# Kernel tuning notes

Measured on AMD Instinct MI355X. Metric: run time of the kernel, lower is better.

## Reference

```python
import jax, jax.numpy as jnp
import numpy as np

N = 50000      # nodes
E = 800000     # edges (avg degree 16)
D = 128        # feature / channel width (channel_counts=[128,128,128])
HEAD = 64      # head_dim
NEG_SLOPE = 0.2  # PyG GATConv leaky_relu slope


def setup_inputs() -> dict:
    key = jax.random.key(0)
    ks = jax.random.split(key, 32)
    s = 1.0 / np.sqrt(D)

    def w(k, shape):
        return jax.random.normal(k, shape, jnp.float32) * s

    return {
        "x": jax.random.normal(ks[0], (N, D), jnp.float32),
        "edge_index": jax.random.randint(ks[1], (2, E), 0, N, dtype=jnp.int32),
        # layer 0: lazy (-1,-1) GATConv -> separate src/dst linear maps
        "w0_src": w(ks[2], (D, D)), "w0_dst": w(ks[3], (D, D)),
        "a0_src": w(ks[4], (D,)), "a0_dst": w(ks[5], (D,)),
        "bc0": jnp.zeros((D,), jnp.float32),
        "wl0": w(ks[6], (D, D)), "bl0": jnp.zeros((D,), jnp.float32),
        # layer 1: int in_channels -> shared weight
        "w1": w(ks[7], (D, D)),
        "a1_src": w(ks[8], (D,)), "a1_dst": w(ks[9], (D,)),
        "bc1": jnp.zeros((D,), jnp.float32),
        "wl1": w(ks[10], (D, D)), "bl1": jnp.zeros((D,), jnp.float32),
        # layer 2
        "w2": w(ks[11], (D, D)),
        "a2_src": w(ks[12], (D,)), "a2_dst": w(ks[13], (D,)),
        "bc2": jnp.zeros((D,), jnp.float32),
        "wl2": w(ks[14], (D, D)), "bl2": jnp.zeros((D,), jnp.float32),
        # head linear
        "wh": w(ks[15], (D, HEAD)), "bh": jnp.zeros((HEAD,), jnp.float32),
    }


def _gat(h_src, h_dst, src, dst, a_src, a_dst, bias):
    """PyG GATConv (heads=1, no self loops, eval-mode). h_*: [N,C]."""
    al_s = h_src @ a_src                                   # [N]
    al_d = h_dst @ a_dst                                   # [N]
    logits = jax.nn.leaky_relu(al_s[src] + al_d[dst], NEG_SLOPE)  # [E]
    m = jax.ops.segment_max(logits, dst, num_segments=N)  # per-dest max
    e = jnp.exp(logits - m[dst])
    denom = jax.ops.segment_sum(e, dst, num_segments=N)
    alpha = e / denom[dst]                                 # [E]
    msg = h_src[src] * alpha[:, None]                      # [E,C]
    return jax.ops.segment_sum(msg, dst, num_segments=N) + bias


def reference(x, edge_index, w0_src, w0_dst, a0_src, a0_dst, bc0, wl0, bl0,
              w1, a1_src, a1_dst, bc1, wl1, bl1,
              w2, a2_src, a2_dst, bc2, wl2, bl2, wh, bh):
    src, dst = edge_index[0], edge_index[1]
    # layer 0: conv(x) + lin(x), relu
    h = _gat(x @ w0_src, x @ w0_dst, src, dst, a0_src, a0_dst, bc0) + x @ wl0 + bl0
    h = jax.nn.relu(h)
    # layer 1: shared-weight conv
    hs = h @ w1
    h = _gat(hs, hs, src, dst, a1_src, a1_dst, bc1) + h @ wl1 + bl1
    h = jax.nn.relu(h)
    # layer 2 (no relu)
    hs = h @ w2
    h = _gat(hs, hs, src, dst, a2_src, a2_dst, bc2) + h @ wl2 + bl2
    # head
    return h @ wh + bh
```

## Files before the change

### kernel.cpp

```cpp
#include <hip/hip_runtime.h>

#define NNODE 50000
#define NEDGE 800000
#define DIM   128
#define NEG   0.2f
#define NBUCK 196
#define EPB1  2048
#define NB1   391
#define GBLK  782
#define GN    12500
#define SB_PA (NB1)
#define SB_PH (SB_PA + 32)
#define SB_MV (SB_PH + 9)
#define SB_CV (SB_MV + 193)
#define SB_TOT (SB_CV + GN)

typedef __attribute__((ext_vector_type(8))) short bf16x8;
typedef __attribute__((ext_vector_type(4))) float f32x4;

__device__ __forceinline__ float wmax(float v){
  #pragma unroll
  for (int m = 32; m > 0; m >>= 1) v = fmaxf(v, __shfl_xor(v, m));
  return v;
}
__device__ __forceinline__ float wsum(float v){
  #pragma unroll
  for (int m = 32; m > 0; m >>= 1) v += __shfl_xor(v, m);
  return v;
}
__device__ __forceinline__ unsigned short f2bf(float f){
  unsigned int x = __float_as_uint(f);
  return (unsigned short)((x + 0x7fffu + ((x >> 16) & 1u)) >> 16);
}
__device__ __forceinline__ float bflo(unsigned u){ return __uint_as_float(u << 16); }
__device__ __forceinline__ float bfhi(unsigned u){ return __uint_as_float(u & 0xffff0000u); }

__global__ __launch_bounds__(256) void setup_k(
    const int* __restrict__ ei,
    const float* __restrict__ x,
    const float* __restrict__ w0s, const float* __restrict__ a0s,
    const float* __restrict__ w0d, const float* __restrict__ a0d,
    const float* __restrict__ bc0, const float* __restrict__ wl0,
    const float* __restrict__ bl0,
    const float* __restrict__ w1,  const float* __restrict__ a1s,
    const float* __restrict__ a1d, const float* __restrict__ bc1,
    const float* __restrict__ wl1, const float* __restrict__ bl1,
    const float* __restrict__ w2,  const float* __restrict__ a2s,
    const float* __restrict__ a2d, const float* __restrict__ bc2,
    const float* __restrict__ wl2, const float* __restrict__ bl2,
    const float* __restrict__ wh,  const float* __restrict__ bh,
    int* __restrict__ cnt,
    unsigned short* __restrict__ Wz1, unsigned short* __restrict__ Wz2,
    unsigned short* __restrict__ Wz3, float* __restrict__ bf3,
    float* __restrict__ uv, float* __restrict__ bf1, float* __restrict__ bf2,
    unsigned int* __restrict__ Xb){
  int bid = blockIdx.x;

  if (bid < NB1){
    __shared__ int h[NBUCK];
    const int* dst = ei + NEDGE;
    for (int i = threadIdx.x; i < NBUCK; i += 256) h[i] = 0;
    __syncthreads();
    int e0 = bid * EPB1 + threadIdx.x;
    #pragma unroll
    for (int i = 0; i < 8; ++i){
      int e = e0 + i * 256;
      if (e < NEDGE) atomicAdd(&h[dst[e] >> 8], 1);
    }
    __syncthreads();
    for (int i = threadIdx.x; i < NBUCK; i += 256)
      cnt[i * NB1 + bid] = h[i];
    return;
  }
  if (bid < SB_PH){
    int g = (bid - SB_PA) * 256 + threadIdx.x;
    int layer = g >> 12;
    int rem = g & 4095;
    int ct = rem >> 9, q = (rem >> 6) & 7, lane = rem & 63;
    int quad = lane >> 4;
    int c = ct * 16 + (lane & 15);
    const float* wA = layer ? w1 : w0s;
    const float* wB = layer ? wl1 : wl0;
    unsigned short* dst = (layer ? Wz2 : Wz1) + ((size_t)(ct * 8 + q) * 64 + lane) * 8;
    #pragma unroll
    for (int j = 0; j < 8; ++j){
      int k = q * 32 + quad * 8 + j;
      float v = (k < 128) ? wA[k * 128 + c] : wB[(k - 128) * 128 + c];
      dst[j] = f2bf(v);
    }
    return;
  }
  if (bid < SB_MV){
    int pb = bid - SB_PH;
    if (pb == 8){
      int c = threadIdx.x;
      if (c < 64){
        float s = bh[c];
        for (int t = 0; t < 128; ++t) s += (bc2[t] + bl2[t]) * wh[t * 64 + c];
        bf3[c] = s;
      }
      return;
    }
    int g = pb * 256 + threadIdx.x;
    int ct = g >> 9, q = (g >> 6) & 7, lane = g & 63;
    int quad = lane >> 4;
    int c = ct * 16 + (lane & 15);
    unsigned short* dst = Wz3 + ((size_t)(ct * 8 + q) * 64 + lane) * 8;
    #pragma unroll
    for (int j = 0; j < 8; ++j){
      int k = q * 32 + quad * 8 + j;
      const float* src = (k < 128) ? (w2 + k * 128) : (wl2 + (k - 128) * 128);
      float s = 0.f;
      for (int t = 0; t < 128; ++t) s += src[t] * wh[t * 64 + c];
      dst[j] = f2bf(s);
    }
    return;
  }
  if (bid < SB_CV){
    int mb = bid - SB_MV;
    if (mb == 192){
      int t = threadIdx.x;
      if (t < 128) bf1[t] = bc0[t] + bl0[t];
      else bf2[t - 128] = bc1[t - 128] + bl1[t - 128];
      return;
    }
    int lane = threadIdx.x & 63;
    int idx = mb * 4 + (threadIdx.x >> 6);
    int grp = idx >> 7, r = idx & 127;
    const float* W; const float* a;
    switch (grp){
      case 0: W = w0s; a = a0s; break;
      case 1: W = w0d; a = a0d; break;
      case 2: W = w1;  a = a1s; break;
      case 3: W = w1;  a = a1d; break;
      case 4: W = w2;  a = a2s; break;
      default: W = w2; a = a2d; break;
    }
    float2 w = ((const float2*)(W + r * DIM))[lane];
    float2 av = ((const float2*)a)[lane];
    float s = wsum(w.x * av.x + w.y * av.y);
    if (lane == 0) uv[grp * 128 + r] = s;
    return;
  }
  {
    int lane = threadIdx.x & 63;
    int n = (bid - SB_CV) * 4 + (threadIdx.x >> 6);
    if (n >= NNODE) return;
    float2 xv = ((const float2*)(x + (size_t)n * DIM))[lane];
    Xb[(size_t)n * 64 + lane] = (unsigned)f2bf(xv.x) | ((unsigned)f2bf(xv.y) << 16);
  }
}

__global__ __launch_bounds__(256) void scan196_k(const int* __restrict__ cnt,
                                                 int* __restrict__ cbase,
                                                 int* __restrict__ btot){
  __shared__ int sd[256];
  int b = blockIdx.x, t = threadIdx.x;
  const int* row = cnt + (size_t)b * NB1;
  int i0 = t * 2, i1 = t * 2 + 1;
  int v0 = (i0 < NB1) ? row[i0] : 0;
  int v1 = (i1 < NB1) ? row[i1] : 0;
  int s = v0 + v1;
  sd[t] = s; __syncthreads();
  #pragma unroll
  for (int off = 1; off < 256; off <<= 1){
    int u = (t >= off) ? sd[t - off] : 0;
    __syncthreads();
    sd[t] += u;
    __syncthreads();
  }
  int ex = sd[t] - s;
  if (i0 < NB1) cbase[(size_t)b * NB1 + i0] = ex;
  if (i1 < NB1) cbase[(size_t)b * NB1 + i1] = ex + v0;
  if (t == 255) btot[b] = sd[255];
}

__global__ __launch_bounds__(256) void bscan2_k(const int* __restrict__ btot,
                                                int* __restrict__ gbase,
                                                int* __restrict__ rp,
                                                const float* __restrict__ X,
                                                const float* __restrict__ uv,
                                                float* __restrict__ als,
                                                float* __restrict__ ald){
  if (blockIdx.x > 0){
    int lane = threadIdx.x & 63;
    int n = (blockIdx.x - 1) * 4 + (threadIdx.x >> 6);
    if (n >= NNODE) return;
    float2 xv = ((const float2*)(X + (size_t)n * DIM))[lane];
    float2 uu = ((const float2*)uv)[lane];
    float2 vv = ((const float2*)(uv + 128))[lane];
    float s1 = wsum(xv.x * uu.x + xv.y * uu.y);
    float s2 = wsum(xv.x * vv.x + xv.y * vv.y);
    if (lane == 0){ als[n] = s1; ald[n] = s2; }
    return;
  }
  __shared__ int sd[256];
  int t = threadIdx.x;
  int v = (t < NBUCK) ? btot[t] : 0;
  sd[t] = v; __syncthreads();
  #pragma unroll
  for (int off = 1; off < 256; off <<= 1){
    int u = (t >= off) ? sd[t - off] : 0;
    __syncthreads();
    sd[t] += u;
    __syncthreads();
  }
  if (t < NBUCK) gbase[t] = sd[t] - v;
  if (t == NBUCK - 1) gbase[NBUCK] = sd[t];
  if (t == 0) rp[NNODE] = NEDGE;
}

__global__ __launch_bounds__(256) void scat2_k(const int* __restrict__ ei,
                                               const int* __restrict__ gbase,
                                               const int* __restrict__ cbase,
                                               unsigned int* __restrict__ packed){
  __shared__ int lcur[NBUCK];
  for (int i = threadIdx.x; i < NBUCK; i += 256) lcur[i] = 0;
  __syncthreads();
  int e0 = blockIdx.x * EPB1 + threadIdx.x;
  #pragma unroll
  for (int i = 0; i < 8; ++i){
    int e = e0 + i * 256;
    if (e < NEDGE){
      int s = ei[e], d = ei[NEDGE + e];
      int b = d >> 8;
      int r = atomicAdd(&lcur[b], 1);
      int pos = gbase[b] + cbase[(size_t)b * NB1 + blockIdx.x] + r;
      packed[pos] = ((unsigned)d << 16) | (unsigned)s;
    }
  }
}

__global__ __launch_bounds__(256) void build_k(const int* __restrict__ gbase,
                                               const unsigned int* __restrict__ packed,
                                               int* __restrict__ rp,
                                               unsigned short* __restrict__ es){
  __shared__ int h[256], sd[256], cur[256];
  int b = blockIdx.x, t = threadIdx.x;
  int s0 = gbase[b], s1 = gbase[b + 1];
  h[t] = 0; __syncthreads();
  for (int i = s0 + t; i < s1; i += 256)
    atomicAdd(&h[(packed[i] >> 16) & 255], 1);
  __syncthreads();
  int v = h[t]; sd[t] = v; __syncthreads();
  #pragma unroll
  for (int off = 1; off < 256; off <<= 1){
    int u = (t >= off) ? sd[t - off] : 0;
    __syncthreads();
    sd[t] += u;
    __syncthreads();
  }
  int ex = sd[t] - v;
  cur[t] = ex;
  int d = b * 256 + t;
  if (d < NNODE) rp[d] = s0 + ex;
  __syncthreads();
  for (int i = s0 + t; i < s1; i += 256){
    unsigned int p = packed[i];
    int ld = (p >> 16) & 255;
    int pos = atomicAdd(&cur[ld], 1);
    es[s0 + pos] = (unsigned short)(p & 0xffffu);
  }
}

__global__ __launch_bounds__(256) void gat_k(const int* __restrict__ rp,
                                             const unsigned short* __restrict__ es,
                                             const float* __restrict__ als,
                                             const float* __restrict__ ald,
                                             const unsigned int* __restrict__ A,
                                             unsigned int* __restrict__ Mb){
  int lane = threadIdx.x & 63;
  int n = blockIdx.x * 4 + (threadIdx.x >> 6);
  if (n >= NNODE) return;
  int start = rp[n], end = rp[n + 1];
  int deg = end - start;
  float ad = ald[n];

  if (deg <= 64){
    int s = 0; float z = -3.0e38f;
    if (lane < deg){
      s = es[start + lane];
      float t = als[s] + ad;
      z = t > 0.f ? t : NEG * t;
    }
    float m = wmax(z);
    float e = (lane < deg) ? __expf(z - m) : 0.f;
    float denom = wsum(e);
    float rinv = (deg > 0) ? 1.f / denom : 0.f;

    int half = lane >> 4;
    int sub  = lane & 15;
    const uint4* A4 = (const uint4*)A;
    float a0 = 0.f, a1 = 0.f, a2 = 0.f, a3 = 0.f;
    float a4 = 0.f, a5 = 0.f, a6 = 0.f, a7 = 0.f;
    int dq = (deg + 7) & ~7;
    for (int j = 0; j < dq; j += 8){
      int   sA = __shfl(s, j + half);
      int   sB = __shfl(s, j + 4 + half);
      float wA = __shfl(e, j + half);
      float wB = __shfl(e, j + 4 + half);
      uint4 pA = A4[(size_t)sA * 16 + sub];
      uint4 pB = A4[(size_t)sB * 16 + sub];
      a0 = fmaf(wA, bflo(pA.x), a0); a1 = fmaf(wA, bfhi(pA.x), a1);
      a2 = fmaf(wA, bflo(pA.y), a2); a3 = fmaf(wA, bfhi(pA.y), a3);
      a4 = fmaf(wA, bflo(pA.z), a4); a5 = fmaf(wA, bfhi(pA.z), a5);
      a6 = fmaf(wA, bflo(pA.w), a6); a7 = fmaf(wA, bfhi(pA.w), a7);
      a0 = fmaf(wB, bflo(pB.x), a0); a1 = fmaf(wB, bfhi(pB.x), a1);
      a2 = fmaf(wB, bflo(pB.y), a2); a3 = fmaf(wB, bfhi(pB.y), a3);
      a4 = fmaf(wB, bflo(pB.z), a4); a5 = fmaf(wB, bfhi(pB.z), a5);
      a6 = fmaf(wB, bflo(pB.w), a6); a7 = fmaf(wB, bfhi(pB.w), a7);
    }
    #define RED(v) v += __shfl_xor(v, 16); v += __shfl_xor(v, 32);
    RED(a0) RED(a1) RED(a2) RED(a3) RED(a4) RED(a5) RED(a6) RED(a7)
    #undef RED
    if (half == 0){
      uint4 o;
      o.x = (unsigned)f2bf(a0 * rinv) | ((unsigned)f2bf(a1 * rinv) << 16);
      o.y = (unsigned)f2bf(a2 * rinv) | ((unsigned)f2bf(a3 * rinv) << 16);
      o.z = (unsigned)f2bf(a4 * rinv) | ((unsigned)f2bf(a5 * rinv) << 16);
      o.w = (unsigned)f2bf(a6 * rinv) | ((unsigned)f2bf(a7 * rinv) << 16);
      ((uint4*)(Mb + (size_t)n * 64))[sub] = o;
    }
  } else {
    float2 acc = make_float2(0.f, 0.f);
    float mloc = -3.0e38f;
    for (int i = start + lane; i < end; i += 64){
      int s = es[i];
      float zz = als[s] + ad;
      zz = zz > 0.f ? zz : NEG * zz;
      mloc = fmaxf(mloc, zz);
    }
    float m = wmax(mloc);
    float dloc = 0.f;
    for (int i = start + lane; i < end; i += 64){
      int s = es[i];
      float zz = als[s] + ad;
      zz = zz > 0.f ? zz : NEG * zz;
      dloc += __expf(zz - m);
    }
    float rinv = 1.f / wsum(dloc);
    for (int i = start; i < end; ++i){
      int s = es[i];
      float zz = als[s] + ad;
      zz = zz > 0.f ? zz : NEG * zz;
      float w = __expf(zz - m);
      unsigned p = A[(size_t)s * 64 + lane];
      acc.x = fmaf(w, bflo(p), acc.x);
      acc.y = fmaf(w, bfhi(p), acc.y);
    }
    Mb[(size_t)n * 64 + lane] =
        (unsigned)f2bf(acc.x * rinv) | ((unsigned)f2bf(acc.y * rinv) << 16);
  }
}

template<int FINAL>
__global__ __launch_bounds__(256) void mfma_k(const unsigned int* __restrict__ Mb,
                                              const unsigned int* __restrict__ Hin,
                                              const unsigned short* __restrict__ Wz,
                                              const float* __restrict__ bias,
                                              const float* __restrict__ u,
                                              const float* __restrict__ v,
                                              unsigned short* __restrict__ Hout,
                                              float* __restrict__ outf,
                                              float* __restrict__ als,
                                              float* __restrict__ ald){
  int lane = threadIdx.x & 63;
  int wid  = threadIdx.x >> 6;
  int r0   = blockIdx.x * 64 + wid * 16;
  int quad = lane >> 4;
  int col  = lane & 15;

  int rA = r0 + col; if (rA > NNODE - 1) rA = NNODE - 1;
  const bf16x8* mrow = (const bf16x8*)(Mb + (size_t)rA * 64);
  const bf16x8* hrow = (const bf16x8*)(Hin + (size_t)rA * 64);
  bf16x8 a[8];
  #pragma unroll
  for (int q = 0; q < 4; ++q){
    a[q]     = mrow[q * 4 + quad];
    a[q + 4] = hrow[q * 4 + quad];
  }

  const bf16x8* wz = (const bf16x8*)Wz;
  int rowq = r0 + quad * 4;
  float alsp[4] = {0.f, 0.f, 0.f, 0.f};
  float aldp[4] = {0.f, 0.f, 0.f, 0.f};
  const int NCT = FINAL ? 4 : 8;

  #pragma unroll
  for (int ct = 0; ct < NCT; ++ct){
    f32x4 acc = {0.f, 0.f, 0.f, 0.f};
    #pragma unroll
    for (int q = 0; q < 8; ++q){
      bf16x8 bfr = wz[(ct * 8 + q) * 64 + lane];
      acc = __builtin_amdgcn_mfma_f32_16x16x32_bf16(a[q], bfr, acc, 0, 0, 0);
    }
    int c = ct * 16 + col;
    float bb = bias[c];
    if (FINAL){
      #pragma unroll
      for (int r = 0; r < 4; ++r){
        int row = rowq + r;
        if (row < NNODE) outf[(size_t)row * 64 + c] = acc[r] + bb;
      }
    } else {
      float uc = u[c], vc = v[c];
      #pragma unroll
      for (int r = 0; r < 4; ++r){
        float h = fmaxf(acc[r] + bb, 0.f);
        alsp[r] = fmaf(h, uc, alsp[r]);
        aldp[r] = fmaf(h, vc, aldp[r]);
        int row = rowq + r;
        if (row < NNODE) Hout[(size_t)row * 128 + c] = f2bf(h);
      }
    }
  }

  if (!FINAL){
    #pragma unroll
    for (int m = 1; m < 16; m <<= 1){
      #pragma unroll
      for (int r = 0; r < 4; ++r){
        alsp[r] += __shfl_xor(alsp[r], m);
        aldp[r] += __shfl_xor(aldp[r], m);
      }
    }
    if (col == 0){
      #pragma unroll
      for (int r = 0; r < 4; ++r){
        int row = rowq + r;
        if (row < NNODE){ als[row] = alsp[r]; ald[row] = aldp[r]; }
      }
    }
  }
}

extern "C" void kernel_launch(void* const* d_in, const int* in_sizes, int n_in,
                              void* d_out, int out_size, void* d_ws, size_t ws_size,
                              hipStream_t stream){
  const float* x   = (const float*)d_in[0];
  const int*   ei  = (const int*)d_in[1];
  const float* w0s = (const float*)d_in[2];
  const float* w0d = (const float*)d_in[3];
  const float* a0s = (const float*)d_in[4];
  const float* a0d = (const float*)d_in[5];
  const float* bc0 = (const float*)d_in[6];
  const float* wl0 = (const float*)d_in[7];
  const float* bl0 = (const float*)d_in[8];
  const float* w1  = (const float*)d_in[9];
  const float* a1s = (const float*)d_in[10];
  const float* a1d = (const float*)d_in[11];
  const float* bc1 = (const float*)d_in[12];
  const float* wl1 = (const float*)d_in[13];
  const float* bl1 = (const float*)d_in[14];
  const float* w2  = (const float*)d_in[15];
  const float* a2s = (const float*)d_in[16];
  const float* a2d = (const float*)d_in[17];
  const float* bc2 = (const float*)d_in[18];
  const float* wl2 = (const float*)d_in[19];
  const float* bl2 = (const float*)d_in[20];
  const float* wh  = (const float*)d_in[21];
  const float* bh  = (const float*)d_in[22];
  float* out = (float*)d_out;

  unsigned int* Xb = (unsigned int*)d_ws;
  unsigned int* Ha = Xb + (size_t)NNODE * 64;
  unsigned int* Hb = Ha + (size_t)NNODE * 64;
  unsigned int* Mb = Hb + (size_t)NNODE * 64;
  float* alsA = (float*)(Mb + (size_t)NNODE * 64);
  float* aldA = alsA + NNODE;
  float* alsB = aldA + NNODE;
  float* aldB = alsB + NNODE;
  float* uv   = aldB + NNODE;
  float* bf1  = uv + 6 * 128;
  float* bf2  = bf1 + 128;
  float* bf3  = bf2 + 128;
  unsigned short* Wz1 = (unsigned short*)(bf3 + 64);
  unsigned short* Wz2 = Wz1 + 256 * 128;
  unsigned short* Wz3 = Wz2 + 256 * 128;
  int*   rp    = (int*)(Wz3 + 256 * 64);
  int*   cnt   = rp + (NNODE + 1);
  int*   cbase = cnt + NBUCK * NB1;
  int*   btot  = cbase + NBUCK * NB1;
  int*   gbase = btot + NBUCK;
  unsigned int* packed = (unsigned int*)(gbase + (NBUCK + 1));
  unsigned short* es   = (unsigned short*)(packed + NEDGE);

  dim3 b(256);
  dim3 gn(GN);

  setup_k<<<SB_TOT, b, 0, stream>>>(ei, x,
      w0s, a0s, w0d, a0d, bc0, wl0, bl0,
      w1, a1s, a1d, bc1, wl1, bl1,
      w2, a2s, a2d, bc2, wl2, bl2, wh, bh,
      cnt, Wz1, Wz2, Wz3, bf3, uv, bf1, bf2, Xb);

  scan196_k<<<NBUCK, b, 0, stream>>>(cnt, cbase, btot);
  bscan2_k<<<1 + GN, b, 0, stream>>>(btot, gbase, rp, x, uv, alsA, aldA);
  scat2_k<<<NB1, b, 0, stream>>>(ei, gbase, cbase, packed);
  build_k<<<NBUCK, b, 0, stream>>>(gbase, packed, rp, es);

  gat_k<<<gn, b, 0, stream>>>(rp, es, alsA, aldA, Xb, Mb);
  mfma_k<0><<<GBLK, b, 0, stream>>>(Mb, Xb, Wz1, bf1, uv + 2 * 128, uv + 3 * 128,
                                    (unsigned short*)Ha, nullptr, alsB, aldB);

  gat_k<<<gn, b, 0, stream>>>(rp, es, alsB, aldB, Ha, Mb);
  mfma_k<0><<<GBLK, b, 0, stream>>>(Mb, Ha, Wz2, bf2, uv + 4 * 128, uv + 5 * 128,
                                    (unsigned short*)Hb, nullptr, alsA, aldA);

  gat_k<<<gn, b, 0, stream>>>(rp, es, alsA, aldA, Hb, Mb);
  mfma_k<1><<<GBLK, b, 0, stream>>>(Mb, Hb, Wz3, bf3, nullptr, nullptr,
                                    nullptr, out, nullptr, nullptr);
}
```

Measured before the change: 307.0 us.

## Split GAT aggregation into alpha pass and column-strip gather with strip-major features

Node features are stored strip-major, as four column strips of 32 bf16 per node, so each strip's gather working set is a quarter of the full feature table. The softmax weights are computed once per layer into a per-edge alpha buffer that reuses the packed scratch area. A new kernel then gathers one strip per block over a four-fold larger grid. The aim is better L2 locality for the random source-row gathers. The cost is an extra kernel launch per layer, four re-reads of edge indices and alpha, and scattered strided writes in the mfma epilogue.

```diff
diff --git a/kernel.cpp b/kernel.cpp
--- a/kernel.cpp
+++ b/kernel.cpp
@@ -9,6 +9,8 @@
 #define NB1   391
 #define GBLK  782
 #define GN    12500
+#define NSTRIP 4
+#define SDW   (NNODE * 16)
 #define SB_PA (NB1)
 #define SB_PH (SB_PA + 32)
 #define SB_MV (SB_PH + 9)
@@ -147,7 +149,8 @@
     int n = (bid - SB_CV) * 4 + (threadIdx.x >> 6);
     if (n >= NNODE) return;
     float2 xv = ((const float2*)(x + (size_t)n * DIM))[lane];
-    Xb[(size_t)n * 64 + lane] = (unsigned)f2bf(xv.x) | ((unsigned)f2bf(xv.y) << 16);
+    unsigned pk = (unsigned)f2bf(xv.x) | ((unsigned)f2bf(xv.y) << 16);
+    Xb[(size_t)(lane >> 4) * SDW + (size_t)n * 16 + (lane & 15)] = pk;
   }
 }
 
@@ -263,66 +266,32 @@
   }
 }
 
-__global__ __launch_bounds__(256) void gat_k(const int* __restrict__ rp,
-                                             const unsigned short* __restrict__ es,
-                                             const float* __restrict__ als,
-                                             const float* __restrict__ ald,
-                                             const unsigned int* __restrict__ A,
-                                             unsigned int* __restrict__ Mb){
+__global__ __launch_bounds__(256) void alpha_k(const int* __restrict__ rp,
+                                               const unsigned short* __restrict__ es,
+                                               const float* __restrict__ als,
+                                               const float* __restrict__ ald,
+                                               float* __restrict__ alpha){
   int lane = threadIdx.x & 63;
   int n = blockIdx.x * 4 + (threadIdx.x >> 6);
   if (n >= NNODE) return;
   int start = rp[n], end = rp[n + 1];
   int deg = end - start;
+  if (deg == 0) return;
   float ad = ald[n];
 
   if (deg <= 64){
-    int s = 0; float z = -3.0e38f;
+    float z = -3.0e38f;
+    int idx = start + lane;
     if (lane < deg){
-      s = es[start + lane];
+      int s = es[idx];
       float t = als[s] + ad;
       z = t > 0.f ? t : NEG * t;
     }
     float m = wmax(z);
     float e = (lane < deg) ? __expf(z - m) : 0.f;
-    float denom = wsum(e);
-    float rinv = (deg > 0) ? 1.f / denom : 0.f;
-
-    int half = lane >> 4;
-    int sub  = lane & 15;
-    const uint4* A4 = (const uint4*)A;
-    float a0 = 0.f, a1 = 0.f, a2 = 0.f, a3 = 0.f;
-    float a4 = 0.f, a5 = 0.f, a6 = 0.f, a7 = 0.f;
-    int dq = (deg + 7) & ~7;
-    for (int j = 0; j < dq; j += 8){
-      int   sA = __shfl(s, j + half);
-      int   sB = __shfl(s, j + 4 + half);
-      float wA = __shfl(e, j + half);
-      float wB = __shfl(e, j + 4 + half);
-      uint4 pA = A4[(size_t)sA * 16 + sub];
-      uint4 pB = A4[(size_t)sB * 16 + sub];
-      a0 = fmaf(wA, bflo(pA.x), a0); a1 = fmaf(wA, bfhi(pA.x), a1);
-      a2 = fmaf(wA, bflo(pA.y), a2); a3 = fmaf(wA, bfhi(pA.y), a3);
-      a4 = fmaf(wA, bflo(pA.z), a4); a5 = fmaf(wA, bfhi(pA.z), a5);
-      a6 = fmaf(wA, bflo(pA.w), a6); a7 = fmaf(wA, bfhi(pA.w), a7);
-      a0 = fmaf(wB, bflo(pB.x), a0); a1 = fmaf(wB, bfhi(pB.x), a1);
-      a2 = fmaf(wB, bflo(pB.y), a2); a3 = fmaf(wB, bfhi(pB.y), a3);
-      a4 = fmaf(wB, bflo(pB.z), a4); a5 = fmaf(wB, bfhi(pB.z), a5);
-      a6 = fmaf(wB, bflo(pB.w), a6); a7 = fmaf(wB, bfhi(pB.w), a7);
-    }
-    #define RED(v) v += __shfl_xor(v, 16); v += __shfl_xor(v, 32);
-    RED(a0) RED(a1) RED(a2) RED(a3) RED(a4) RED(a5) RED(a6) RED(a7)
-    #undef RED
-    if (half == 0){
-      uint4 o;
-      o.x = (unsigned)f2bf(a0 * rinv) | ((unsigned)f2bf(a1 * rinv) << 16);
-      o.y = (unsigned)f2bf(a2 * rinv) | ((unsigned)f2bf(a3 * rinv) << 16);
-      o.z = (unsigned)f2bf(a4 * rinv) | ((unsigned)f2bf(a5 * rinv) << 16);
-      o.w = (unsigned)f2bf(a6 * rinv) | ((unsigned)f2bf(a7 * rinv) << 16);
-      ((uint4*)(Mb + (size_t)n * 64))[sub] = o;
-    }
+    float rinv = 1.f / wsum(e);
+    if (lane < deg) alpha[idx] = e * rinv;
   } else {
-    float2 acc = make_float2(0.f, 0.f);
     float mloc = -3.0e38f;
     for (int i = start + lane; i < end; i += 64){
       int s = es[i];
@@ -339,18 +308,48 @@
       dloc += __expf(zz - m);
     }
     float rinv = 1.f / wsum(dloc);
-    for (int i = start; i < end; ++i){
+    for (int i = start + lane; i < end; i += 64){
       int s = es[i];
       float zz = als[s] + ad;
       zz = zz > 0.f ? zz : NEG * zz;
-      float w = __expf(zz - m);
-      unsigned p = A[(size_t)s * 64 + lane];
-      acc.x = fmaf(w, bflo(p), acc.x);
-      acc.y = fmaf(w, bfhi(p), acc.y);
-    }
-    Mb[(size_t)n * 64 + lane] =
-        (unsigned)f2bf(acc.x * rinv) | ((unsigned)f2bf(acc.y * rinv) << 16);
-  }
+      alpha[i] = __expf(zz - m) * rinv;
+    }
+  }
+}
+
+__global__ __launch_bounds__(256) void mgat_k(const int* __restrict__ rp,
+                                              const unsigned short* __restrict__ es,
+                                              const float* __restrict__ alpha,
+                                              const unsigned int* __restrict__ A,
+                                              unsigned int* __restrict__ Mb){
+  int bid = blockIdx.x;
+  int strip = bid / GN;
+  int nb = bid - strip * GN;
+  int lane = threadIdx.x & 63;
+  int n = nb * 4 + (threadIdx.x >> 6);
+  if (n >= NNODE) return;
+  int start = rp[n], end = rp[n + 1];
+  int half = lane >> 4, sub = lane & 15;
+  const unsigned int* As = A + (size_t)strip * SDW;
+  float ax = 0.f, ay = 0.f;
+
+  for (int j = start; j < end; j += 8){
+    int i0 = j + half, i1 = j + 4 + half;
+    bool v0 = i0 < end, v1 = i1 < end;
+    int s0 = v0 ? es[i0] : 0;
+    int s1 = v1 ? es[i1] : 0;
+    float w0 = v0 ? alpha[i0] : 0.f;
+    float w1 = v1 ? alpha[i1] : 0.f;
+    unsigned p0 = As[(size_t)s0 * 16 + sub];
+    unsigned p1 = As[(size_t)s1 * 16 + sub];
+    ax = fmaf(w0, bflo(p0), ax); ay = fmaf(w0, bfhi(p0), ay);
+    ax = fmaf(w1, bflo(p1), ax); ay = fmaf(w1, bfhi(p1), ay);
+  }
+  ax += __shfl_xor(ax, 16); ax += __shfl_xor(ax, 32);
+  ay += __shfl_xor(ay, 16); ay += __shfl_xor(ay, 32);
+  if (half == 0)
+    Mb[(size_t)strip * SDW + (size_t)n * 16 + sub] =
+        (unsigned)f2bf(ax) | ((unsigned)f2bf(ay) << 16);
 }
 
 template<int FINAL>
@@ -371,13 +370,13 @@
   int col  = lane & 15;
 
   int rA = r0 + col; if (rA > NNODE - 1) rA = NNODE - 1;
-  const bf16x8* mrow = (const bf16x8*)(Mb + (size_t)rA * 64);
-  const bf16x8* hrow = (const bf16x8*)(Hin + (size_t)rA * 64);
+  const unsigned int* mb = Mb  + (size_t)rA * 16 + quad * 4;
+  const unsigned int* hb = Hin + (size_t)rA * 16 + quad * 4;
   bf16x8 a[8];
   #pragma unroll
   for (int q = 0; q < 4; ++q){
-    a[q]     = mrow[q * 4 + quad];
-    a[q + 4] = hrow[q * 4 + quad];
+    a[q]     = *(const bf16x8*)(mb + (size_t)q * SDW);
+    a[q + 4] = *(const bf16x8*)(hb + (size_t)q * SDW);
   }
 
   const bf16x8* wz = (const bf16x8*)Wz;
@@ -410,7 +409,8 @@
         alsp[r] = fmaf(h, uc, alsp[r]);
         aldp[r] = fmaf(h, vc, aldp[r]);
         int row = rowq + r;
-        if (row < NNODE) Hout[(size_t)row * 128 + c] = f2bf(h);
+        if (row < NNODE)
+          Hout[(size_t)(c >> 5) * (NNODE * 32) + (size_t)row * 32 + (c & 31)] = f2bf(h);
       }
     }
   }
@@ -484,9 +484,11 @@
   int*   gbase = btot + NBUCK;
   unsigned int* packed = (unsigned int*)(gbase + (NBUCK + 1));
   unsigned short* es   = (unsigned short*)(packed + NEDGE);
+  float* alpha = (float*)packed;
 
   dim3 b(256);
   dim3 gn(GN);
+  dim3 gs(NSTRIP * GN);
 
   setup_k<<<SB_TOT, b, 0, stream>>>(ei, x,
       w0s, a0s, w0d, a0d, bc0, wl0, bl0,
@@ -499,15 +501,18 @@
   scat2_k<<<NB1, b, 0, stream>>>(ei, gbase, cbase, packed);
   build_k<<<NBUCK, b, 0, stream>>>(gbase, packed, rp, es);
 
-  gat_k<<<gn, b, 0, stream>>>(rp, es, alsA, aldA, Xb, Mb);
+  alpha_k<<<gn, b, 0, stream>>>(rp, es, alsA, aldA, alpha);
+  mgat_k<<<gs, b, 0, stream>>>(rp, es, alpha, Xb, Mb);
   mfma_k<0><<<GBLK, b, 0, stream>>>(Mb, Xb, Wz1, bf1, uv + 2 * 128, uv + 3 * 128,
                                     (unsigned short*)Ha, nullptr, alsB, aldB);
 
-  gat_k<<<gn, b, 0, stream>>>(rp, es, alsB, aldB, Ha, Mb);
+  alpha_k<<<gn, b, 0, stream>>>(rp, es, alsB, aldB, alpha);
+  mgat_k<<<gs, b, 0, stream>>>(rp, es, alpha, Ha, Mb);
   mfma_k<0><<<GBLK, b, 0, stream>>>(Mb, Ha, Wz2, bf2, uv + 4 * 128, uv + 5 * 128,
                                     (unsigned short*)Hb, nullptr, alsA, aldA);
 
-  gat_k<<<gn, b, 0, stream>>>(rp, es, alsA, aldA, Hb, Mb);
+  alpha_k<<<gn, b, 0, stream>>>(rp, es, alsA, aldA, alpha);
+  mgat_k<<<gs, b, 0, stream>>>(rp, es, alpha, Hb, Mb);
   mfma_k<1><<<GBLK, b, 0, stream>>>(Mb, Hb, Wz3, bf3, nullptr, nullptr,
                                     nullptr, out, nullptr, nullptr);
 }
```

Result: slower. 499.0 us (+62.5%).

## Fuse GAT aggregation into MFMA transform kernel via swizzled LDS staging

Applied to the files above, without the earlier changes.

Merges the per-node attention aggregation kernel into the following MFMA linear kernel. Each wave now aggregates its 16 rows, writes the bf16 results into XOR-swizzled shared memory, and reads them back as MFMA A fragments, so the Mb intermediate no longer goes through global memory and three launches disappear. In exchange the grid drops from 12500 to 782 blocks, and each wave handles 16 nodes one after another. This cuts parallelism available for hiding gather latency and may worsen load imbalance.

```diff
diff --git a/kernel.cpp b/kernel.cpp
--- a/kernel.cpp
+++ b/kernel.cpp
@@ -263,120 +263,110 @@
   }
 }
 
-__global__ __launch_bounds__(256) void gat_k(const int* __restrict__ rp,
-                                             const unsigned short* __restrict__ es,
-                                             const float* __restrict__ als,
-                                             const float* __restrict__ ald,
-                                             const unsigned int* __restrict__ A,
-                                             unsigned int* __restrict__ Mb){
-  int lane = threadIdx.x & 63;
-  int n = blockIdx.x * 4 + (threadIdx.x >> 6);
-  if (n >= NNODE) return;
-  int start = rp[n], end = rp[n + 1];
-  int deg = end - start;
-  float ad = ald[n];
-
-  if (deg <= 64){
-    int s = 0; float z = -3.0e38f;
-    if (lane < deg){
-      s = es[start + lane];
-      float t = als[s] + ad;
-      z = t > 0.f ? t : NEG * t;
-    }
-    float m = wmax(z);
-    float e = (lane < deg) ? __expf(z - m) : 0.f;
-    float denom = wsum(e);
-    float rinv = (deg > 0) ? 1.f / denom : 0.f;
-
-    int half = lane >> 4;
-    int sub  = lane & 15;
-    const uint4* A4 = (const uint4*)A;
-    float a0 = 0.f, a1 = 0.f, a2 = 0.f, a3 = 0.f;
-    float a4 = 0.f, a5 = 0.f, a6 = 0.f, a7 = 0.f;
-    int dq = (deg + 7) & ~7;
-    for (int j = 0; j < dq; j += 8){
-      int   sA = __shfl(s, j + half);
-      int   sB = __shfl(s, j + 4 + half);
-      float wA = __shfl(e, j + half);
-      float wB = __shfl(e, j + 4 + half);
-      uint4 pA = A4[(size_t)sA * 16 + sub];
-      uint4 pB = A4[(size_t)sB * 16 + sub];
-      a0 = fmaf(wA, bflo(pA.x), a0); a1 = fmaf(wA, bfhi(pA.x), a1);
-      a2 = fmaf(wA, bflo(pA.y), a2); a3 = fmaf(wA, bfhi(pA.y), a3);
-      a4 = fmaf(wA, bflo(pA.z), a4); a5 = fmaf(wA, bfhi(pA.z), a5);
-      a6 = fmaf(wA, bflo(pA.w), a6); a7 = fmaf(wA, bfhi(pA.w), a7);
-      a0 = fmaf(wB, bflo(pB.x), a0); a1 = fmaf(wB, bfhi(pB.x), a1);
-      a2 = fmaf(wB, bflo(pB.y), a2); a3 = fmaf(wB, bfhi(pB.y), a3);
-      a4 = fmaf(wB, bflo(pB.z), a4); a5 = fmaf(wB, bfhi(pB.z), a5);
-      a6 = fmaf(wB, bflo(pB.w), a6); a7 = fmaf(wB, bfhi(pB.w), a7);
-    }
-    #define RED(v) v += __shfl_xor(v, 16); v += __shfl_xor(v, 32);
-    RED(a0) RED(a1) RED(a2) RED(a3) RED(a4) RED(a5) RED(a6) RED(a7)
-    #undef RED
-    if (half == 0){
-      uint4 o;
-      o.x = (unsigned)f2bf(a0 * rinv) | ((unsigned)f2bf(a1 * rinv) << 16);
-      o.y = (unsigned)f2bf(a2 * rinv) | ((unsigned)f2bf(a3 * rinv) << 16);
-      o.z = (unsigned)f2bf(a4 * rinv) | ((unsigned)f2bf(a5 * rinv) << 16);
-      o.w = (unsigned)f2bf(a6 * rinv) | ((unsigned)f2bf(a7 * rinv) << 16);
-      ((uint4*)(Mb + (size_t)n * 64))[sub] = o;
-    }
-  } else {
-    float2 acc = make_float2(0.f, 0.f);
-    float mloc = -3.0e38f;
-    for (int i = start + lane; i < end; i += 64){
-      int s = es[i];
-      float zz = als[s] + ad;
-      zz = zz > 0.f ? zz : NEG * zz;
-      mloc = fmaxf(mloc, zz);
-    }
-    float m = wmax(mloc);
-    float dloc = 0.f;
-    for (int i = start + lane; i < end; i += 64){
-      int s = es[i];
-      float zz = als[s] + ad;
-      zz = zz > 0.f ? zz : NEG * zz;
-      dloc += __expf(zz - m);
-    }
-    float rinv = 1.f / wsum(dloc);
-    for (int i = start; i < end; ++i){
-      int s = es[i];
-      float zz = als[s] + ad;
-      zz = zz > 0.f ? zz : NEG * zz;
-      float w = __expf(zz - m);
-      unsigned p = A[(size_t)s * 64 + lane];
-      acc.x = fmaf(w, bflo(p), acc.x);
-      acc.y = fmaf(w, bfhi(p), acc.y);
-    }
-    Mb[(size_t)n * 64 + lane] =
-        (unsigned)f2bf(acc.x * rinv) | ((unsigned)f2bf(acc.y * rinv) << 16);
-  }
-}
-
 template<int FINAL>
-__global__ __launch_bounds__(256) void mfma_k(const unsigned int* __restrict__ Mb,
-                                              const unsigned int* __restrict__ Hin,
-                                              const unsigned short* __restrict__ Wz,
-                                              const float* __restrict__ bias,
-                                              const float* __restrict__ u,
-                                              const float* __restrict__ v,
-                                              unsigned short* __restrict__ Hout,
-                                              float* __restrict__ outf,
-                                              float* __restrict__ als,
-                                              float* __restrict__ ald){
+__global__ __launch_bounds__(256) void fused_k(
+    const int* __restrict__ rp, const unsigned short* __restrict__ es,
+    const float* __restrict__ alsi, const float* __restrict__ aldi,
+    const unsigned int* __restrict__ A,
+    const unsigned int* __restrict__ Hin,
+    const unsigned short* __restrict__ Wz,
+    const float* __restrict__ bias,
+    const float* __restrict__ u, const float* __restrict__ v,
+    unsigned short* __restrict__ Hout, float* __restrict__ outf,
+    float* __restrict__ also, float* __restrict__ aldo){
+  __shared__ unsigned int lds[64 * 64];
   int lane = threadIdx.x & 63;
   int wid  = threadIdx.x >> 6;
   int r0   = blockIdx.x * 64 + wid * 16;
-  int quad = lane >> 4;
-  int col  = lane & 15;
-
+  int half = lane >> 4, sub = lane & 15;
+  const uint4* A4 = (const uint4*)A;
+  uint4* lds4 = (uint4*)lds;
+
+  for (int i = 0; i < 16; ++i){
+    int n = r0 + i;
+    if (n >= NNODE) break;
+    int start = rp[n], end = rp[n + 1];
+    int deg = end - start;
+    float ad = aldi[n];
+    if (deg <= 64){
+      int s = 0; float z = -3.0e38f;
+      if (lane < deg){
+        s = es[start + lane];
+        float t = alsi[s] + ad;
+        z = t > 0.f ? t : NEG * t;
+      }
+      float m = wmax(z);
+      float e = (lane < deg) ? __expf(z - m) : 0.f;
+      float denom = wsum(e);
+      float rinv = (deg > 0) ? 1.f / denom : 0.f;
+      float a0=0.f,a1=0.f,a2=0.f,a3=0.f,a4=0.f,a5=0.f,a6=0.f,a7=0.f;
+      int dq = (deg + 7) & ~7;
+      for (int j = 0; j < dq; j += 8){
+        int   sA = __shfl(s, j + half);
+        int   sB = __shfl(s, j + 4 + half);
+        float wA = __shfl(e, j + half);
+        float wB = __shfl(e, j + 4 + half);
+        uint4 pA = A4[(size_t)sA * 16 + sub];
+        uint4 pB = A4[(size_t)sB * 16 + sub];
+        a0 = fmaf(wA, bflo(pA.x), a0); a1 = fmaf(wA, bfhi(pA.x), a1);
+        a2 = fmaf(wA, bflo(pA.y), a2); a3 = fmaf(wA, bfhi(pA.y), a3);
+        a4 = fmaf(wA, bflo(pA.z), a4); a5 = fmaf(wA, bfhi(pA.z), a5);
+        a6 = fmaf(wA, bflo(pA.w), a6); a7 = fmaf(wA, bfhi(pA.w), a7);
+        a0 = fmaf(wB, bflo(pB.x), a0); a1 = fmaf(wB, bfhi(pB.x), a1);
+        a2 = fmaf(wB, bflo(pB.y), a2); a3 = fmaf(wB, bfhi(pB.y), a3);
+        a4 = fmaf(wB, bflo(pB.z), a4); a5 = fmaf(wB, bfhi(pB.z), a5);
+        a6 = fmaf(wB, bflo(pB.w), a6); a7 = fmaf(wB, bfhi(pB.w), a7);
+      }
+      #define RED(vv) vv += __shfl_xor(vv, 16); vv += __shfl_xor(vv, 32);
+      RED(a0) RED(a1) RED(a2) RED(a3) RED(a4) RED(a5) RED(a6) RED(a7)
+      #undef RED
+      if (half == 0){
+        uint4 o;
+        o.x = (unsigned)f2bf(a0 * rinv) | ((unsigned)f2bf(a1 * rinv) << 16);
+        o.y = (unsigned)f2bf(a2 * rinv) | ((unsigned)f2bf(a3 * rinv) << 16);
+        o.z = (unsigned)f2bf(a4 * rinv) | ((unsigned)f2bf(a5 * rinv) << 16);
+        o.w = (unsigned)f2bf(a6 * rinv) | ((unsigned)f2bf(a7 * rinv) << 16);
+        lds4[(wid * 16 + i) * 16 + (sub ^ (i & 7))] = o;
+      }
+    } else {
+      float mloc = -3.0e38f;
+      for (int it = start + lane; it < end; it += 64){
+        int s = es[it];
+        float zz = alsi[s] + ad;
+        zz = zz > 0.f ? zz : NEG * zz;
+        mloc = fmaxf(mloc, zz);
+      }
+      float m = wmax(mloc);
+      float dloc = 0.f;
+      for (int it = start + lane; it < end; it += 64){
+        int s = es[it];
+        float zz = alsi[s] + ad;
+        zz = zz > 0.f ? zz : NEG * zz;
+        dloc += __expf(zz - m);
+      }
+      float rinv = 1.f / wsum(dloc);
+      float ax = 0.f, ay = 0.f;
+      for (int it = start; it < end; ++it){
+        int s = es[it];
+        float zz = alsi[s] + ad;
+        zz = zz > 0.f ? zz : NEG * zz;
+        float w = __expf(zz - m);
+        unsigned p = A[(size_t)s * 64 + lane];
+        ax = fmaf(w, bflo(p), ax);
+        ay = fmaf(w, bfhi(p), ay);
+      }
+      lds[(wid * 16 + i) * 64 + (lane ^ ((i & 7) << 2))] =
+          (unsigned)f2bf(ax * rinv) | ((unsigned)f2bf(ay * rinv) << 16);
+    }
+  }
+
+  int quad = half, col = sub;
   int rA = r0 + col; if (rA > NNODE - 1) rA = NNODE - 1;
-  const bf16x8* mrow = (const bf16x8*)(Mb + (size_t)rA * 64);
   const bf16x8* hrow = (const bf16x8*)(Hin + (size_t)rA * 64);
   bf16x8 a[8];
   #pragma unroll
   for (int q = 0; q < 4; ++q){
-    a[q]     = mrow[q * 4 + quad];
+    a[q]     = *(const bf16x8*)&lds4[(wid * 16 + col) * 16 + ((q * 4 + quad) ^ (col & 7))];
     a[q + 4] = hrow[q * 4 + quad];
   }
 
@@ -428,7 +418,7 @@
       #pragma unroll
       for (int r = 0; r < 4; ++r){
         int row = rowq + r;
-        if (row < NNODE){ als[row] = alsp[r]; ald[row] = aldp[r]; }
+        if (row < NNODE){ also[row] = alsp[r]; aldo[row] = aldp[r]; }
       }
     }
   }
@@ -486,7 +476,6 @@
   unsigned short* es   = (unsigned short*)(packed + NEDGE);
 
   dim3 b(256);
-  dim3 gn(GN);
 
   setup_k<<<SB_TOT, b, 0, stream>>>(ei, x,
       w0s, a0s, w0d, a0d, bc0, wl0, bl0,
@@ -499,15 +488,15 @@
   scat2_k<<<NB1, b, 0, stream>>>(ei, gbase, cbase, packed);
   build_k<<<NBUCK, b, 0, stream>>>(gbase, packed, rp, es);
 
-  gat_k<<<gn, b, 0, stream>>>(rp, es, alsA, aldA, Xb, Mb);
-  mfma_k<0><<<GBLK, b, 0, stream>>>(Mb, Xb, Wz1, bf1, uv + 2 * 128, uv + 3 * 128,
-                                    (unsigned short*)Ha, nullptr, alsB, aldB);
-
-  gat_k<<<gn, b, 0, stream>>>(rp, es, alsB, aldB, Ha, Mb);
-  mfma_k<0><<<GBLK, b, 0, stream>>>(Mb, Ha, Wz2, bf2, uv + 4 * 128, uv + 5 * 128,
-                                    (unsigned short*)Hb, nullptr, alsA, aldA);
-
-  gat_k<<<gn, b, 0, stream>>>(rp, es, alsA, aldA, Hb, Mb);
-  mfma_k<1><<<GBLK, b, 0, stream>>>(Mb, Hb, Wz3, bf3, nullptr, nullptr,
-                                    nullptr, out, nullptr, nullptr);
-}
+  fused_k<0><<<GBLK, b, 0, stream>>>(rp, es, alsA, aldA, Xb, Xb, Wz1, bf1,
+                                     uv + 2 * 128, uv + 3 * 128,
+                                     (unsigned short*)Ha, nullptr, alsB, aldB);
+
+  fused_k<0><<<GBLK, b, 0, stream>>>(rp, es, alsB, aldB, Ha, Ha, Wz2, bf2,
+                                     uv + 4 * 128, uv + 5 * 128,
+                                     (unsigned short*)Hb, nullptr, alsA, aldA);
+
+  fused_k<1><<<GBLK, b, 0, stream>>>(rp, es, alsA, aldA, Hb, Hb, Wz3, bf3,
+                                     nullptr, nullptr, nullptr, out,
+                                     nullptr, nullptr);
+}
```

Measured after the change: 343.4 us. +11.9%, slower.
